# Kernel tuning notes

Measured on AMD Instinct MI355X. Metric: run time of the kernel, lower is better.

Reference implementation:

```python
import jax, jax.numpy as jnp
import numpy as np

N = 50000      # nodes
E = 800000     # edges (before self-loops)
F_IN = 128     # num_features
HID = 32       # hidden channels per head (conv1)
HEADS = 4      # conv1 heads
C = 40         # classes (conv2 out channels)
OUT_HEADS = 1  # conv2 heads
NEG_SLOPE = 0.2


def setup_inputs() -> dict:
    key = jax.random.key(0)
    ks = jax.random.split(key, 10)
    x = jax.random.normal(ks[0], (N, F_IN), jnp.float32)
    edge_index = jax.random.randint(ks[1], (2, E), 0, N, jnp.int32)
    s1 = 1.0 / np.sqrt(F_IN).astype(np.float32)
    s1h = 1.0 / np.sqrt(HID).astype(np.float32)
    s2 = 1.0 / np.sqrt(HEADS * HID).astype(np.float32)
    s2c = 1.0 / np.sqrt(C).astype(np.float32)
    W1 = jax.random.normal(ks[2], (F_IN, HEADS * HID), jnp.float32) * s1
    att_src1 = jax.random.normal(ks[3], (HEADS, HID), jnp.float32) * s1h
    att_dst1 = jax.random.normal(ks[4], (HEADS, HID), jnp.float32) * s1h
    bias1 = jnp.zeros((HEADS * HID,), jnp.float32)
    W2 = jax.random.normal(ks[5], (HEADS * HID, OUT_HEADS * C), jnp.float32) * s2
    att_src2 = jax.random.normal(ks[6], (OUT_HEADS, C), jnp.float32) * s2c
    att_dst2 = jax.random.normal(ks[7], (OUT_HEADS, C), jnp.float32) * s2c
    bias2 = jnp.zeros((C,), jnp.float32)
    return {"x": x, "edge_index": edge_index,
            "W1": W1, "att_src1": att_src1, "att_dst1": att_dst1, "bias1": bias1,
            "W2": W2, "att_src2": att_src2, "att_dst2": att_dst2, "bias2": bias2}


def gat_layer(h_in, src, dst, W, a_src, a_dst, bias, heads, out_ch, concat):
    """PyG GATConv (v1) in inference mode (no dropout on attention)."""
    n = h_in.shape[0]
    h = (h_in @ W).reshape(n, heads, out_ch)              # [N,H,F]
    e_src = jnp.einsum('nhf,hf->nh', h, a_src)            # [N,H]
    e_dst = jnp.einsum('nhf,hf->nh', h, a_dst)            # [N,H]
    alpha = jax.nn.leaky_relu(e_src[src] + e_dst[dst], NEG_SLOPE)  # [E,H]
    # segment softmax over destination-node neighborhoods
    amax = jax.ops.segment_max(alpha, dst, num_segments=n)
    amax = jnp.where(jnp.isfinite(amax), amax, 0.0)
    ex = jnp.exp(alpha - amax[dst])
    denom = jax.ops.segment_sum(ex, dst, num_segments=n)
    coef = ex / (denom[dst] + 1e-16)                      # [E,H]
    # scatter-aggregate weighted source messages
    out = jax.ops.segment_sum(h[src] * coef[:, :, None], dst, num_segments=n)  # [N,H,F]
    out = out.reshape(n, heads * out_ch) if concat else out.mean(axis=1)
    return out + bias


def reference(x, edge_index, W1, att_src1, att_dst1, bias1, W2, att_src2, att_dst2, bias2):
    n = x.shape[0]
    loop = jnp.arange(n, dtype=edge_index.dtype)          # GATConv adds self-loops
    src = jnp.concatenate([edge_index[0], loop])
    dst = jnp.concatenate([edge_index[1], loop])
    h = jax.nn.elu(gat_layer(x, src, dst, W1, att_src1, att_dst1, bias1, HEADS, HID, True))
    out = gat_layer(h, src, dst, W2, att_src2, att_dst2, bias2, OUT_HEADS, C, False)
    return (jax.nn.log_softmax(out, axis=1), jax.nn.softmax(out, axis=1))
```

## Files before the change

kernel.cpp:

```cpp
#include <hip/hip_runtime.h>
#include <hip/hip_bf16.h>

#define F1   128
#define H1   4
#define C2   40
#define NEG  0.2f
#define DS   96

typedef __hip_bfloat16 bf16;
typedef float f32x2 __attribute__((ext_vector_type(2)));
typedef short s16x8 __attribute__((ext_vector_type(8)));
typedef float f32x4 __attribute__((ext_vector_type(4)));

__device__ __forceinline__ float ldf(const void* p, size_t i, int isbf) {
    return isbf ? __bfloat162float(((const bf16*)p)[i]) : ((const float*)p)[i];
}
__device__ __forceinline__ float lrelu(float a) { return a > 0.f ? a : NEG * a; }

__device__ __forceinline__ unsigned short f2bfb(float f, float& back) {
    unsigned u = __float_as_uint(f);
    unsigned r = u + 0x7FFFu + ((u >> 16) & 1u);
    unsigned short h = (unsigned short)(r >> 16);
    back = __uint_as_float((unsigned)h << 16);
    return h;
}

__device__ __forceinline__ void up2(unsigned g, float& lo, float& hi) {
    lo = __uint_as_float(g << 16);
    hi = __uint_as_float(g & 0xffff0000u);
}
__device__ __forceinline__ f32x2 up2v(unsigned g) {
    f32x2 r;
    r.x = __uint_as_float(g << 16);
    r.y = __uint_as_float(g & 0xffff0000u);
    return r;
}

__global__ void k_prep(const unsigned short* __restrict__ x, int* __restrict__ deg,
                       int N, int* __restrict__ flag) {
    int i = blockIdx.x * 256 + threadIdx.x;
    if (i < N) deg[i] = 0;
    if (blockIdx.x == 0) {
        __shared__ int sh[256];
        int cnt = 0;
        for (int k = threadIdx.x; k < 8192; k += 256)
            if (((x[k] >> 7) & 0xFF) >= 160) cnt++;
        sh[threadIdx.x] = cnt;
        __syncthreads();
        for (int s = 128; s > 0; s >>= 1) {
            if (threadIdx.x < s) sh[threadIdx.x] += sh[threadIdx.x + s];
            __syncthreads();
        }
        if (threadIdx.x == 0) flag[0] = (sh[0] < 100) ? 1 : 0;
    }
}

__global__ void k_wprep(const void* __restrict__ W1, const int* __restrict__ flag,
                        unsigned short* __restrict__ w1t_hi,
                        unsigned short* __restrict__ w1t_lo) {
    int idx = blockIdx.x * 256 + threadIdx.x;
    int k = idx >> 7, c = idx & 127;
    const int isbf = flag[0];
    float v = ldf(W1, idx, isbf);
    float back;
    unsigned short hi = f2bfb(v, back);
    float d2;
    unsigned short lo = f2bfb(v - back, d2);
    w1t_hi[c * 128 + k] = hi;
    w1t_lo[c * 128 + k] = isbf ? (unsigned short)0 : lo;
}

__global__ void __launch_bounds__(256) k_scat(const int* __restrict__ ei, int E, int ET,
                                              int* __restrict__ deg,
                                              int* __restrict__ ebuf2) {
    int e = blockIdx.x * 256 + threadIdx.x;
    if (e >= ET) return;
    int s, d;
    if (e < E) { s = ei[e]; d = ei[E + e]; }
    else       { s = e - E; d = e - E; }
    int pos = atomicAdd(&deg[d], 1);
    if (pos < DS) ebuf2[d * DS + pos] = s;
}

__global__ void __launch_bounds__(256) k_gemm1(
        const void* __restrict__ x, const unsigned short* __restrict__ w1t_hi,
        const unsigned short* __restrict__ w1t_lo,
        const void* __restrict__ as1, const void* __restrict__ ad1,
        const int* __restrict__ flag,
        bf16* __restrict__ h1b, float* __restrict__ es1, float* __restrict__ ed1,
        int N) {
    const int isbf = flag[0];
    int t = threadIdx.x, wv = t >> 6, l = t & 63;
    int r0 = (wv & 1) * 16, c0 = (wv >> 1) * 64;
    int lr = l & 15, q = l >> 4;
    int n0 = blockIdx.x * 32;
    int rowa = n0 + r0 + lr; if (rowa >= N) rowa = N - 1;

    const bf16*  xb = (const bf16*)x;
    const float* xf = (const float*)x;
    f32x4 acc[4] = {};

#pragma unroll
    for (int ks = 0; ks < 4; ks++) {
        int kb = ks * 32 + q * 8;
        s16x8 ahi, alo;
        if (isbf) {
            ahi = *(const s16x8*)&xb[(size_t)rowa * 128 + kb];
        } else {
            const float* xr = xf + (size_t)rowa * 128 + kb;
            float4 v0 = *(const float4*)xr;
            float4 v1 = *(const float4*)(xr + 4);
            float vv[8] = {v0.x, v0.y, v0.z, v0.w, v1.x, v1.y, v1.z, v1.w};
#pragma unroll
            for (int j = 0; j < 8; j++) {
                float back;
                unsigned short hb = f2bfb(vv[j], back);
                float d2;
                unsigned short lb = f2bfb(vv[j] - back, d2);
                ahi[j] = (short)hb;
                alo[j] = (short)lb;
            }
        }
#pragma unroll
        for (int f = 0; f < 4; f++) {
            int col = c0 + f * 16 + lr;
            s16x8 bh = *(const s16x8*)&w1t_hi[(size_t)col * 128 + kb];
            acc[f] = __builtin_amdgcn_mfma_f32_16x16x32_bf16(ahi, bh, acc[f], 0, 0, 0);
            if (!isbf) {
                s16x8 bl = *(const s16x8*)&w1t_lo[(size_t)col * 128 + kb];
                acc[f] = __builtin_amdgcn_mfma_f32_16x16x32_bf16(alo, bh, acc[f], 0, 0, 0);
                acc[f] = __builtin_amdgcn_mfma_f32_16x16x32_bf16(ahi, bl, acc[f], 0, 0, 0);
            }
        }
    }

    float asv[4], adv[4];
#pragma unroll
    for (int f = 0; f < 4; f++) {
        asv[f] = ldf(as1, c0 + f * 16 + lr, isbf);
        adv[f] = ldf(ad1, c0 + f * 16 + lr, isbf);
    }
    float ps0[4], ps1[4], pd0[4], pd1[4];
#pragma unroll
    for (int r = 0; r < 4; r++) {
        int rw = n0 + r0 + q * 4 + r;
        ps0[r] = acc[0][r] * asv[0] + acc[1][r] * asv[1];
        ps1[r] = acc[2][r] * asv[2] + acc[3][r] * asv[3];
        pd0[r] = acc[0][r] * adv[0] + acc[1][r] * adv[1];
        pd1[r] = acc[2][r] * adv[2] + acc[3][r] * adv[3];
        if (rw < N) {
#pragma unroll
            for (int f = 0; f < 4; f++)
                h1b[(size_t)rw * 128 + c0 + f * 16 + lr] = __float2bfloat16(acc[f][r]);
        }
    }
#pragma unroll
    for (int off = 1; off < 16; off <<= 1) {
#pragma unroll
        for (int r = 0; r < 4; r++) {
            ps0[r] += __shfl_xor(ps0[r], off, 64);
            ps1[r] += __shfl_xor(ps1[r], off, 64);
            pd0[r] += __shfl_xor(pd0[r], off, 64);
            pd1[r] += __shfl_xor(pd1[r], off, 64);
        }
    }
    if (lr == 0) {
        int h0 = c0 >> 5;
#pragma unroll
        for (int r = 0; r < 4; r++) {
            int rw = n0 + r0 + q * 4 + r;
            if (rw < N) {
                es1[rw * H1 + h0]     = ps0[r];
                es1[rw * H1 + h0 + 1] = ps1[r];
                ed1[rw * H1 + h0]     = pd0[r];
                ed1[rw * H1 + h0 + 1] = pd1[r];
            }
        }
    }
}

__global__ void __launch_bounds__(256) k_l1(
        const int* __restrict__ deg, const int* __restrict__ ebuf2,
        const float* __restrict__ es1, const float* __restrict__ ed1,
        const uint4* __restrict__ h1p4, const void* __restrict__ b1,
        const void* __restrict__ W2, const void* __restrict__ as2,
        const void* __restrict__ ad2, const int* __restrict__ flag,
        bf16* __restrict__ h2b, float* __restrict__ es2, float* __restrict__ ed2,
        int N) {
    int w = threadIdx.x >> 6, l = threadIdx.x & 63;
    int d = blockIdx.x * 4 + w; if (d >= N) d = N - 1;
    int cnt = deg[d]; if (cnt > DS) cnt = DS;
    int start = d * DS;

    __shared__ int   s_sh[4][DS];
    __shared__ float ev_sh[4][4][DS + 4];
    __shared__ float hs[4][144];

    float4 edv = *(const float4*)&ed1[(size_t)d * 4];
    float t0 = 0.f, t1 = 0.f, t2 = 0.f, t3 = 0.f;
    if (l < cnt) {
        int s = ebuf2[start + l];
        s_sh[w][l] = s;
        float4 es4 = *(const float4*)&es1[(size_t)s * 4];
        float v0 = __expf(lrelu(es4.x + edv.x));
        float v1 = __expf(lrelu(es4.y + edv.y));
        float v2 = __expf(lrelu(es4.z + edv.z));
        float v3 = __expf(lrelu(es4.w + edv.w));
        ev_sh[w][0][l] = v0; ev_sh[w][1][l] = v1;
        ev_sh[w][2][l] = v2; ev_sh[w][3][l] = v3;
        t0 = v0; t1 = v1; t2 = v2; t3 = v3;
    }
    if (cnt > 64) {
        int l2 = 64 + l;
        if (l2 < cnt) {
            int s = ebuf2[start + l2];
            s_sh[w][l2] = s;
            float4 es4 = *(const float4*)&es1[(size_t)s * 4];
            float v0 = __expf(lrelu(es4.x + edv.x));
            float v1 = __expf(lrelu(es4.y + edv.y));
            float v2 = __expf(lrelu(es4.z + edv.z));
            float v3 = __expf(lrelu(es4.w + edv.w));
            ev_sh[w][0][l2] = v0; ev_sh[w][1][l2] = v1;
            ev_sh[w][2][l2] = v2; ev_sh[w][3][l2] = v3;
            t0 += v0; t1 += v1; t2 += v2; t3 += v3;
        }
    }
#pragma unroll
    for (int off = 32; off > 0; off >>= 1) {
        t0 += __shfl_xor(t0, off, 64);
        t1 += __shfl_xor(t1, off, 64);
        t2 += __shfl_xor(t2, off, 64);
        t3 += __shfl_xor(t3, off, 64);
    }
    __syncthreads();

    int q = l >> 4, c16 = l & 15, h = c16 >> 2;
    f32x2 acc[4] = {{0.f, 0.f}, {0.f, 0.f}, {0.f, 0.f}, {0.f, 0.f}};
    for (int i = 0; i < cnt; i += 16) {
#pragma unroll
        for (int u = 0; u < 4; u++) {
            int e = i + q + 4 * u;
            int ec = min(e, cnt - 1);
            float evh = (e < cnt) ? ev_sh[w][h][ec] : 0.f;
            int s = s_sh[w][ec];
            uint4 g = h1p4[(size_t)s * 16 + c16];
            f32x2 ev2 = {evh, evh};
            acc[0] += ev2 * up2v(g.x);
            acc[1] += ev2 * up2v(g.y);
            acc[2] += ev2 * up2v(g.z);
            acc[3] += ev2 * up2v(g.w);
        }
    }

#pragma unroll
    for (int off = 16; off <= 32; off <<= 1) {
#pragma unroll
        for (int jj = 0; jj < 4; jj++) {
            acc[jj].x += __shfl_xor(acc[jj].x, off, 64);
            acc[jj].y += __shfl_xor(acc[jj].y, off, 64);
        }
    }

    const int isbf = flag[0];
    float dsum = (h == 0) ? t0 : (h == 1) ? t1 : (h == 2) ? t2 : t3;
    if (q == 0) {
        float inv = 1.f / (dsum + 1e-16f);
#pragma unroll
        for (int j = 0; j < 8; j++) {
            int col = c16 * 8 + j;
            float av = (j & 1) ? acc[j >> 1].y : acc[j >> 1].x;
            float v = av * inv + ldf(b1, col, isbf);
            hs[w][col + (col >> 3)] = v > 0.f ? v : (__expf(v) - 1.f);
        }
    }
    __syncthreads();
    float a2 = 0.f;
    if (l < C2) {
        if (isbf) {
            const bf16* W = (const bf16*)W2;
#pragma unroll 8
            for (int k = 0; k < F1; k++)
                a2 = fmaf(hs[w][k + (k >> 3)], __bfloat162float(W[(size_t)k * C2 + l]), a2);
        } else {
            const float* W = (const float*)W2;
#pragma unroll 8
            for (int k = 0; k < F1; k++)
                a2 = fmaf(hs[w][k + (k >> 3)], W[(size_t)k * C2 + l], a2);
        }
        h2b[(size_t)d * C2 + l] = __float2bfloat16(a2);
    }
    float ps = (l < C2) ? a2 * ldf(as2, l, isbf) : 0.f;
    float pd = (l < C2) ? a2 * ldf(ad2, l, isbf) : 0.f;
#pragma unroll
    for (int off = 32; off > 0; off >>= 1) {
        ps += __shfl_xor(ps, off, 64);
        pd += __shfl_xor(pd, off, 64);
    }
    if (l == 0) { es2[d] = ps; ed2[d] = pd; }
}

__global__ void __launch_bounds__(256) k_l2(
        const int* __restrict__ deg, const int* __restrict__ ebuf2,
        const float* __restrict__ es2, const float* __restrict__ ed2,
        const unsigned* __restrict__ h2p, const void* __restrict__ b2,
        const int* __restrict__ flag, void* __restrict__ out, int N) {
    int w = threadIdx.x >> 6, l = threadIdx.x & 63;
    int d = blockIdx.x * 4 + w; if (d >= N) d = N - 1;
    int cnt = deg[d]; if (cnt > DS) cnt = DS;
    int start = d * DS;
    float edd = ed2[d];

    __shared__ int   s_sh2[4][DS];
    __shared__ float x_sh[4][DS];

    float xv = 0.f;
    if (l < cnt) {
        int s = ebuf2[start + l];
        s_sh2[w][l] = s;
        xv = __expf(lrelu(es2[s] + edd));
        x_sh[w][l] = xv;
    }
    float dsum = xv;
    if (cnt > 64) {
        int l2 = 64 + l;
        if (l2 < cnt) {
            int s = ebuf2[start + l2];
            s_sh2[w][l2] = s;
            float x2 = __expf(lrelu(es2[s] + edd));
            x_sh[w][l2] = x2;
            dsum += x2;
        }
    }
#pragma unroll
    for (int off = 32; off > 0; off >>= 1) dsum += __shfl_xor(dsum, off, 64);
    __syncthreads();

    int half = l >> 5, j = l & 31;
    float acc0 = 0.f, acc1 = 0.f;
    if (j < 20) {
        for (int i = 0; i < cnt; i += 16) {
#pragma unroll
            for (int u = 0; u < 8; u++) {
                int e = i + half * 8 + u;
                int ec = min(e, cnt - 1);
                float x = (e < cnt) ? x_sh[w][ec] : 0.f;
                int s = s_sh2[w][ec];
                unsigned g = h2p[(size_t)s * 20 + j];
                float lo, hi; up2(g, lo, hi);
                acc0 = fmaf(x, lo, acc0);
                acc1 = fmaf(x, hi, acc1);
            }
        }
        acc0 += __shfl_xor(acc0, 32, 64);
        acc1 += __shfl_xor(acc1, 32, 64);
    }

    const int isbf = flag[0];
    float inv = 1.f / (dsum + 1e-16f);
    float v0 = -1e30f, v1 = -1e30f;
    if (l < 20) {
        v0 = acc0 * inv + ldf(b2, 2 * l, isbf);
        v1 = acc1 * inv + ldf(b2, 2 * l + 1, isbf);
    }
    float m = fmaxf(v0, v1);
#pragma unroll
    for (int off = 16; off > 0; off >>= 1) m = fmaxf(m, __shfl_xor(m, off, 32));
    float sv = (l < 20) ? __expf(v0 - m) + __expf(v1 - m) : 0.f;
#pragma unroll
    for (int off = 16; off > 0; off >>= 1) sv += __shfl_xor(sv, off, 32);
    float lse = m + __logf(sv);
    if (l < 20) {
        float ls0 = v0 - lse, ls1 = v1 - lse;
        size_t base = (size_t)d * C2 + 2 * l, halfo = (size_t)N * C2;
        if (isbf) {
            bf16* o = (bf16*)out;
            o[base] = __float2bfloat16(ls0);
            o[base + 1] = __float2bfloat16(ls1);
            o[halfo + base] = __float2bfloat16(__expf(ls0));
            o[halfo + base + 1] = __float2bfloat16(__expf(ls1));
        } else {
            float* o = (float*)out;
            o[base] = ls0;
            o[base + 1] = ls1;
            o[halfo + base] = __expf(ls0);
            o[halfo + base + 1] = __expf(ls1);
        }
    }
}

extern "C" void kernel_launch(void* const* d_in, const int* in_sizes, int n_in,
                              void* d_out, int out_size, void* d_ws, size_t ws_size,
                              hipStream_t stream) {
    const int N  = in_sizes[0] / F1;
    const int E  = in_sizes[1] / 2;
    const int ET = E + N;
    const int NB = (N + 255) / 256;

    const void* x   = d_in[0];
    const int*  ei  = (const int*)d_in[1];
    const void* W1  = d_in[2];
    const void* as1 = d_in[3];
    const void* ad1 = d_in[4];
    const void* b1  = d_in[5];
    const void* W2  = d_in[6];
    const void* as2 = d_in[7];
    const void* ad2 = d_in[8];
    const void* b2  = d_in[9];

    float* ws = (float*)d_ws;
    auto al4 = [](size_t v) { return (v + 3) & ~(size_t)3; };
    size_t o = 0;
    bf16*  h1b  = (bf16*)(ws + o); o = al4(o + (size_t)64 * N);
    float* es1  = ws + o; o = al4(o + (size_t)H1 * N);
    float* ed1  = ws + o; o = al4(o + (size_t)H1 * N);
    bf16*  h2b  = (bf16*)(ws + o); o = al4(o + (size_t)20 * N);
    float* es2  = ws + o; o = al4(o + N);
    float* ed2  = ws + o; o = al4(o + N);
    int*   deg  = (int*)(ws + o); o = al4(o + N);
    int*   flag = (int*)(ws + o); o = al4(o + 4);
    int*   ebuf2 = (int*)(ws + o); o = al4(o + (size_t)DS * N);
    unsigned short* w1t_hi = (unsigned short*)(ws + o); o = al4(o + 8192);
    unsigned short* w1t_lo = (unsigned short*)(ws + o); o = al4(o + 8192);

    k_prep<<<NB, 256, 0, stream>>>((const unsigned short*)x, deg, N, flag);
    k_wprep<<<64, 256, 0, stream>>>(W1, flag, w1t_hi, w1t_lo);
    k_scat<<<(ET + 255) / 256, 256, 0, stream>>>(ei, E, ET, deg, ebuf2);
    k_gemm1<<<(N + 31) / 32, 256, 0, stream>>>(x, w1t_hi, w1t_lo, as1, ad1, flag,
                                               h1b, es1, ed1, N);
    k_l1<<<(N + 3) / 4, 256, 0, stream>>>(deg, ebuf2, es1, ed1, (const uint4*)h1b,
                                          b1, W2, as2, ad2, flag, h2b, es2, ed2, N);
    k_l2<<<(N + 3) / 4, 256, 0, stream>>>(deg, ebuf2, es2, ed2, (const unsigned*)h2b,
                                          b2, flag, d_out, N);
}
```

Measured before the change: 313.2 us.

## Fuse edge scatter into GEMM1 and split adjacency buckets into four sub-copies

The standalone edge-bucketing kernel is folded into the start of the first GEMM kernel, with each block handling a contiguous slice of edges. Per-destination counters and bucket storage are replicated four ways, indexed by block id, to reduce atomic contention on shared counters. The layer kernels gather neighbors by concatenating the four sub-buckets, each capped at 32 entries. This removes a launch and spreads atomics, but the GEMM now waits on scattered atomics, and the 32-per-copy cap could drop edges for high-degree nodes that the old 96 cap kept.

```diff
diff --git a/kernel.cpp b/kernel.cpp
--- a/kernel.cpp
+++ b/kernel.cpp
@@ -6,6 +6,8 @@
 #define C2   40
 #define NEG  0.2f
 #define DS   96
+#define NC   4
+#define DSX  32
 
 typedef __hip_bfloat16 bf16;
 typedef float f32x2 __attribute__((ext_vector_type(2)));
@@ -36,10 +38,10 @@
     return r;
 }
 
-__global__ void k_prep(const unsigned short* __restrict__ x, int* __restrict__ deg,
-                       int N, int* __restrict__ flag) {
+__global__ void k_prep(const unsigned short* __restrict__ x, int* __restrict__ deg_x,
+                       int N4, int* __restrict__ flag) {
     int i = blockIdx.x * 256 + threadIdx.x;
-    if (i < N) deg[i] = 0;
+    if (i < N4) deg_x[i] = 0;
     if (blockIdx.x == 0) {
         __shared__ int sh[256];
         int cnt = 0;
@@ -70,25 +72,28 @@
     w1t_lo[c * 128 + k] = isbf ? (unsigned short)0 : lo;
 }
 
-__global__ void __launch_bounds__(256) k_scat(const int* __restrict__ ei, int E, int ET,
-                                              int* __restrict__ deg,
-                                              int* __restrict__ ebuf2) {
-    int e = blockIdx.x * 256 + threadIdx.x;
-    if (e >= ET) return;
-    int s, d;
-    if (e < E) { s = ei[e]; d = ei[E + e]; }
-    else       { s = e - E; d = e - E; }
-    int pos = atomicAdd(&deg[d], 1);
-    if (pos < DS) ebuf2[d * DS + pos] = s;
-}
-
 __global__ void __launch_bounds__(256) k_gemm1(
         const void* __restrict__ x, const unsigned short* __restrict__ w1t_hi,
         const unsigned short* __restrict__ w1t_lo,
         const void* __restrict__ as1, const void* __restrict__ ad1,
-        const int* __restrict__ flag,
+        const int* __restrict__ flag, const int* __restrict__ ei,
+        int E, int ET, int* __restrict__ deg_x, int* __restrict__ ebufx,
         bf16* __restrict__ h1b, float* __restrict__ es1, float* __restrict__ ed1,
         int N) {
+    {
+        int per = (ET + gridDim.x - 1) / gridDim.x;
+        int he0 = blockIdx.x * per;
+        int he1 = he0 + per; if (he1 > ET) he1 = ET;
+        int xc = blockIdx.x & (NC - 1);
+        for (int e = he0 + threadIdx.x; e < he1; e += 256) {
+            int s, d;
+            if (e < E) { s = ei[e]; d = ei[E + e]; }
+            else       { s = e - E; d = e - E; }
+            size_t seg = (size_t)xc * N + d;
+            int pos = atomicAdd(&deg_x[seg], 1);
+            if (pos < DSX) ebufx[seg * DSX + pos] = s;
+        }
+    }
     const int isbf = flag[0];
     int t = threadIdx.x, wv = t >> 6, l = t & 63;
     int r0 = (wv & 1) * 16, c0 = (wv >> 1) * 64;
@@ -180,7 +185,7 @@
 }
 
 __global__ void __launch_bounds__(256) k_l1(
-        const int* __restrict__ deg, const int* __restrict__ ebuf2,
+        const int* __restrict__ deg_x, const int* __restrict__ ebufx,
         const float* __restrict__ es1, const float* __restrict__ ed1,
         const uint4* __restrict__ h1p4, const void* __restrict__ b1,
         const void* __restrict__ W2, const void* __restrict__ as2,
@@ -189,48 +194,40 @@
         int N) {
     int w = threadIdx.x >> 6, l = threadIdx.x & 63;
     int d = blockIdx.x * 4 + w; if (d >= N) d = N - 1;
-    int cnt = deg[d]; if (cnt > DS) cnt = DS;
-    int start = d * DS;
-
     __shared__ int   s_sh[4][DS];
     __shared__ float ev_sh[4][4][DS + 4];
     __shared__ float hs[4][144];
 
     float4 edv = *(const float4*)&ed1[(size_t)d * 4];
     float t0 = 0.f, t1 = 0.f, t2 = 0.f, t3 = 0.f;
-    if (l < cnt) {
-        int s = ebuf2[start + l];
-        s_sh[w][l] = s;
-        float4 es4 = *(const float4*)&es1[(size_t)s * 4];
-        float v0 = __expf(lrelu(es4.x + edv.x));
-        float v1 = __expf(lrelu(es4.y + edv.y));
-        float v2 = __expf(lrelu(es4.z + edv.z));
-        float v3 = __expf(lrelu(es4.w + edv.w));
-        ev_sh[w][0][l] = v0; ev_sh[w][1][l] = v1;
-        ev_sh[w][2][l] = v2; ev_sh[w][3][l] = v3;
-        t0 = v0; t1 = v1; t2 = v2; t3 = v3;
-    }
-    if (cnt > 64) {
-        int l2 = 64 + l;
-        if (l2 < cnt) {
-            int s = ebuf2[start + l2];
-            s_sh[w][l2] = s;
+    int off = 0;
+#pragma unroll
+    for (int xc = 0; xc < NC; xc++) {
+        size_t seg = (size_t)xc * N + d;
+        int c = deg_x[seg]; if (c > DSX) c = DSX;
+        int take = c; if (off + take > DS) take = DS - off;
+        if (l < take) {
+            int s = ebufx[seg * DSX + l];
+            int idx = off + l;
+            s_sh[w][idx] = s;
             float4 es4 = *(const float4*)&es1[(size_t)s * 4];
             float v0 = __expf(lrelu(es4.x + edv.x));
             float v1 = __expf(lrelu(es4.y + edv.y));
             float v2 = __expf(lrelu(es4.z + edv.z));
             float v3 = __expf(lrelu(es4.w + edv.w));
-            ev_sh[w][0][l2] = v0; ev_sh[w][1][l2] = v1;
-            ev_sh[w][2][l2] = v2; ev_sh[w][3][l2] = v3;
+            ev_sh[w][0][idx] = v0; ev_sh[w][1][idx] = v1;
+            ev_sh[w][2][idx] = v2; ev_sh[w][3][idx] = v3;
             t0 += v0; t1 += v1; t2 += v2; t3 += v3;
         }
-    }
-#pragma unroll
-    for (int off = 32; off > 0; off >>= 1) {
-        t0 += __shfl_xor(t0, off, 64);
-        t1 += __shfl_xor(t1, off, 64);
-        t2 += __shfl_xor(t2, off, 64);
-        t3 += __shfl_xor(t3, off, 64);
+        off += take;
+    }
+    int cnt = off;
+#pragma unroll
+    for (int o = 32; o > 0; o >>= 1) {
+        t0 += __shfl_xor(t0, o, 64);
+        t1 += __shfl_xor(t1, o, 64);
+        t2 += __shfl_xor(t2, o, 64);
+        t3 += __shfl_xor(t3, o, 64);
     }
     __syncthreads();
 
@@ -253,11 +250,11 @@
     }
 
 #pragma unroll
-    for (int off = 16; off <= 32; off <<= 1) {
+    for (int o = 16; o <= 32; o <<= 1) {
 #pragma unroll
         for (int jj = 0; jj < 4; jj++) {
-            acc[jj].x += __shfl_xor(acc[jj].x, off, 64);
-            acc[jj].y += __shfl_xor(acc[jj].y, off, 64);
+            acc[jj].x += __shfl_xor(acc[jj].x, o, 64);
+            acc[jj].y += __shfl_xor(acc[jj].y, o, 64);
         }
     }
 
@@ -292,47 +289,45 @@
     float ps = (l < C2) ? a2 * ldf(as2, l, isbf) : 0.f;
     float pd = (l < C2) ? a2 * ldf(ad2, l, isbf) : 0.f;
 #pragma unroll
-    for (int off = 32; off > 0; off >>= 1) {
-        ps += __shfl_xor(ps, off, 64);
-        pd += __shfl_xor(pd, off, 64);
+    for (int o = 32; o > 0; o >>= 1) {
+        ps += __shfl_xor(ps, o, 64);
+        pd += __shfl_xor(pd, o, 64);
     }
     if (l == 0) { es2[d] = ps; ed2[d] = pd; }
 }
 
 __global__ void __launch_bounds__(256) k_l2(
-        const int* __restrict__ deg, const int* __restrict__ ebuf2,
+        const int* __restrict__ deg_x, const int* __restrict__ ebufx,
         const float* __restrict__ es2, const float* __restrict__ ed2,
         const unsigned* __restrict__ h2p, const void* __restrict__ b2,
         const int* __restrict__ flag, void* __restrict__ out, int N) {
     int w = threadIdx.x >> 6, l = threadIdx.x & 63;
     int d = blockIdx.x * 4 + w; if (d >= N) d = N - 1;
-    int cnt = deg[d]; if (cnt > DS) cnt = DS;
-    int start = d * DS;
     float edd = ed2[d];
 
     __shared__ int   s_sh2[4][DS];
     __shared__ float x_sh[4][DS];
 
-    float xv = 0.f;
-    if (l < cnt) {
-        int s = ebuf2[start + l];
-        s_sh2[w][l] = s;
-        xv = __expf(lrelu(es2[s] + edd));
-        x_sh[w][l] = xv;
-    }
-    float dsum = xv;
-    if (cnt > 64) {
-        int l2 = 64 + l;
-        if (l2 < cnt) {
-            int s = ebuf2[start + l2];
-            s_sh2[w][l2] = s;
-            float x2 = __expf(lrelu(es2[s] + edd));
-            x_sh[w][l2] = x2;
-            dsum += x2;
-        }
-    }
-#pragma unroll
-    for (int off = 32; off > 0; off >>= 1) dsum += __shfl_xor(dsum, off, 64);
+    float dsum = 0.f;
+    int off = 0;
+#pragma unroll
+    for (int xc = 0; xc < NC; xc++) {
+        size_t seg = (size_t)xc * N + d;
+        int c = deg_x[seg]; if (c > DSX) c = DSX;
+        int take = c; if (off + take > DS) take = DS - off;
+        if (l < take) {
+            int s = ebufx[seg * DSX + l];
+            int idx = off + l;
+            s_sh2[w][idx] = s;
+            float xv = __expf(lrelu(es2[s] + edd));
+            x_sh[w][idx] = xv;
+            dsum += xv;
+        }
+        off += take;
+    }
+    int cnt = off;
+#pragma unroll
+    for (int o = 32; o > 0; o >>= 1) dsum += __shfl_xor(dsum, o, 64);
     __syncthreads();
 
     int half = l >> 5, j = l & 31;
@@ -364,10 +359,10 @@
     }
     float m = fmaxf(v0, v1);
 #pragma unroll
-    for (int off = 16; off > 0; off >>= 1) m = fmaxf(m, __shfl_xor(m, off, 32));
+    for (int o = 16; o > 0; o >>= 1) m = fmaxf(m, __shfl_xor(m, o, 32));
     float sv = (l < 20) ? __expf(v0 - m) + __expf(v1 - m) : 0.f;
 #pragma unroll
-    for (int off = 16; off > 0; off >>= 1) sv += __shfl_xor(sv, off, 32);
+    for (int o = 16; o > 0; o >>= 1) sv += __shfl_xor(sv, o, 32);
     float lse = m + __logf(sv);
     if (l < 20) {
         float ls0 = v0 - lse, ls1 = v1 - lse;
@@ -394,7 +389,8 @@
     const int N  = in_sizes[0] / F1;
     const int E  = in_sizes[1] / 2;
     const int ET = E + N;
-    const int NB = (N + 255) / 256;
+    const int N4 = NC * N;
+    const int NB4 = (N4 + 255) / 256;
 
     const void* x   = d_in[0];
     const int*  ei  = (const int*)d_in[1];
@@ -416,19 +412,19 @@
     bf16*  h2b  = (bf16*)(ws + o); o = al4(o + (size_t)20 * N);
     float* es2  = ws + o; o = al4(o + N);
     float* ed2  = ws + o; o = al4(o + N);
-    int*   deg  = (int*)(ws + o); o = al4(o + N);
+    int*   deg_x = (int*)(ws + o); o = al4(o + (size_t)NC * N);
     int*   flag = (int*)(ws + o); o = al4(o + 4);
-    int*   ebuf2 = (int*)(ws + o); o = al4(o + (size_t)DS * N);
+    int*   ebufx = (int*)(ws + o); o = al4(o + (size_t)NC * DSX * N);
     unsigned short* w1t_hi = (unsigned short*)(ws + o); o = al4(o + 8192);
     unsigned short* w1t_lo = (unsigned short*)(ws + o); o = al4(o + 8192);
 
-    k_prep<<<NB, 256, 0, stream>>>((const unsigned short*)x, deg, N, flag);
+    k_prep<<<NB4, 256, 0, stream>>>((const unsigned short*)x, deg_x, N4, flag);
     k_wprep<<<64, 256, 0, stream>>>(W1, flag, w1t_hi, w1t_lo);
-    k_scat<<<(ET + 255) / 256, 256, 0, stream>>>(ei, E, ET, deg, ebuf2);
     k_gemm1<<<(N + 31) / 32, 256, 0, stream>>>(x, w1t_hi, w1t_lo, as1, ad1, flag,
+                                               ei, E, ET, deg_x, ebufx,
                                                h1b, es1, ed1, N);
-    k_l1<<<(N + 3) / 4, 256, 0, stream>>>(deg, ebuf2, es1, ed1, (const uint4*)h1b,
+    k_l1<<<(N + 3) / 4, 256, 0, stream>>>(deg_x, ebufx, es1, ed1, (const uint4*)h1b,
                                           b1, W2, as2, ad2, flag, h2b, es2, ed2, N);
-    k_l2<<<(N + 3) / 4, 256, 0, stream>>>(deg, ebuf2, es2, ed2, (const unsigned*)h2b,
+    k_l2<<<(N + 3) / 4, 256, 0, stream>>>(deg_x, ebufx, es2, ed2, (const unsigned*)h2b,
                                           b2, flag, d_out, N);
 }
```

Measured after the change: 344.8 us. 10.1% more time.

## Replace atomic per-node edge scatter with two-pass binned counting sort into CSR

Applied to the files above, without the earlier changes.

Replaces the global-atomic scatter of edges into fixed 96-slot per-node buckets with a two-pass sort. The first pass bins edges by destination block of 256 nodes, staging them in shared memory. The second pass sorts each bin by local destination in shared memory and writes compact CSR source lists with row starts and degrees. The aim is to cut global atomic contention and scattered writes, and to give the aggregation kernels a denser CSR layout. In exchange it adds an extra kernel and a staging buffer, and edges are silently dropped if a bin exceeds its fixed capacity.

```diff
diff --git a/kernel.cpp b/kernel.cpp
--- a/kernel.cpp
+++ b/kernel.cpp
@@ -6,6 +6,8 @@
 #define C2   40
 #define NEG  0.2f
 #define DS   96
+#define EPB  6400
+#define BCAP 5632
 
 typedef __hip_bfloat16 bf16;
 typedef float f32x2 __attribute__((ext_vector_type(2)));
@@ -36,23 +38,36 @@
     return r;
 }
 
-__global__ void k_prep(const unsigned short* __restrict__ x, int* __restrict__ deg,
-                       int N, int* __restrict__ flag) {
-    int i = blockIdx.x * 256 + threadIdx.x;
-    if (i < N) deg[i] = 0;
-    if (blockIdx.x == 0) {
-        __shared__ int sh[256];
-        int cnt = 0;
-        for (int k = threadIdx.x; k < 8192; k += 256)
-            if (((x[k] >> 7) & 0xFF) >= 160) cnt++;
-        sh[threadIdx.x] = cnt;
+__device__ __forceinline__ int excl_scan256(int v, int t, int* wsum) {
+    int lane = t & 63, wid = t >> 6;
+    int orig = v;
+#pragma unroll
+    for (int o = 1; o < 64; o <<= 1) {
+        int n = __shfl_up(v, o, 64);
+        if (lane >= o) v += n;
+    }
+    if (lane == 63) wsum[wid] = v;
+    __syncthreads();
+    int add = 0;
+    for (int k = 0; k < wid; k++) add += wsum[k];
+    return v + add - orig;
+}
+
+__global__ void k_prep(const unsigned short* __restrict__ x, int* __restrict__ gbin_cnt,
+                       int* __restrict__ flag) {
+    int t = threadIdx.x;
+    gbin_cnt[t] = 0;
+    __shared__ int sh[256];
+    int cnt = 0;
+    for (int k = t; k < 8192; k += 256)
+        if (((x[k] >> 7) & 0xFF) >= 160) cnt++;
+    sh[t] = cnt;
+    __syncthreads();
+    for (int s = 128; s > 0; s >>= 1) {
+        if (t < s) sh[t] += sh[t + s];
         __syncthreads();
-        for (int s = 128; s > 0; s >>= 1) {
-            if (threadIdx.x < s) sh[threadIdx.x] += sh[threadIdx.x + s];
-            __syncthreads();
-        }
-        if (threadIdx.x == 0) flag[0] = (sh[0] < 100) ? 1 : 0;
-    }
+    }
+    if (t == 0) flag[0] = (sh[0] < 100) ? 1 : 0;
 }
 
 __global__ void k_wprep(const void* __restrict__ W1, const int* __restrict__ flag,
@@ -70,16 +85,74 @@
     w1t_lo[c * 128 + k] = isbf ? (unsigned short)0 : lo;
 }
 
-__global__ void __launch_bounds__(256) k_scat(const int* __restrict__ ei, int E, int ET,
-                                              int* __restrict__ deg,
-                                              int* __restrict__ ebuf2) {
-    int e = blockIdx.x * 256 + threadIdx.x;
-    if (e >= ET) return;
-    int s, d;
-    if (e < E) { s = ei[e]; d = ei[E + e]; }
-    else       { s = e - E; d = e - E; }
-    int pos = atomicAdd(&deg[d], 1);
-    if (pos < DS) ebuf2[d * DS + pos] = s;
+__global__ void __launch_bounds__(256) k_scatA(
+        const int* __restrict__ ei, int E, int ET, int nbins,
+        int* __restrict__ gbin_cnt, unsigned long long* __restrict__ stg) {
+    __shared__ int hist[256], lstart[256], gbase[256], lcnt[256];
+    __shared__ int wsum[4];
+    __shared__ unsigned long long stgl[EPB];
+    int t = threadIdx.x;
+    hist[t] = 0; lcnt[t] = 0;
+    __syncthreads();
+    int e0 = blockIdx.x * EPB;
+    int e1 = e0 + EPB; if (e1 > ET) e1 = ET;
+    for (int e = e0 + t; e < e1; e += 256) {
+        int d = (e < E) ? ei[E + e] : (e - E);
+        atomicAdd(&hist[d >> 8], 1);
+    }
+    __syncthreads();
+    if (t < nbins && hist[t] > 0) gbase[t] = atomicAdd(&gbin_cnt[t], hist[t]);
+    int ls = excl_scan256(hist[t], t, wsum);
+    lstart[t] = ls;
+    __syncthreads();
+    for (int e = e0 + t; e < e1; e += 256) {
+        int s, d;
+        if (e < E) { s = ei[e]; d = ei[E + e]; }
+        else       { s = e - E; d = e - E; }
+        int b = d >> 8;
+        int r = atomicAdd(&lcnt[b], 1);
+        stgl[lstart[b] + r] = ((unsigned long long)(unsigned)d << 32) | (unsigned)s;
+    }
+    __syncthreads();
+    int cntb = e1 - e0;
+    for (int i = t; i < cntb; i += 256) {
+        unsigned long long p = stgl[i];
+        int d = (int)(p >> 32);
+        int b = d >> 8;
+        int off = gbase[b] + (i - lstart[b]);
+        if (off < BCAP) stg[(size_t)b * BCAP + off] = p;
+    }
+}
+
+__global__ void __launch_bounds__(256) k_scatB(
+        const unsigned long long* __restrict__ stg, const int* __restrict__ gbin_cnt,
+        int N, int* __restrict__ csr_s, int* __restrict__ rowstart,
+        int* __restrict__ deg) {
+    __shared__ int dhist[256], dstart[256], dcnt[256];
+    __shared__ int wsum[4];
+    __shared__ int out_s[BCAP];
+    int bin = blockIdx.x, t = threadIdx.x;
+    int cnt = gbin_cnt[bin]; if (cnt > BCAP) cnt = BCAP;
+    dhist[t] = 0; dcnt[t] = 0;
+    __syncthreads();
+    const unsigned long long* mystg = stg + (size_t)bin * BCAP;
+    for (int i = t; i < cnt; i += 256)
+        atomicAdd(&dhist[(int)(mystg[i] >> 32) & 255], 1);
+    __syncthreads();
+    int ds = excl_scan256(dhist[t], t, wsum);
+    dstart[t] = ds;
+    __syncthreads();
+    for (int i = t; i < cnt; i += 256) {
+        unsigned long long p = mystg[i];
+        int ld = (int)(p >> 32) & 255;
+        int r = atomicAdd(&dcnt[ld], 1);
+        out_s[dstart[ld] + r] = (int)(p & 0xffffffffu);
+    }
+    __syncthreads();
+    size_t gb = (size_t)bin * BCAP;
+    for (int i = t; i < cnt; i += 256) csr_s[gb + i] = out_s[i];
+    int d = bin * 256 + t;
+    if (d < N) { rowstart[d] = (int)gb + dstart[t]; deg[d] = dhist[t]; }
 }
 
 __global__ void __launch_bounds__(256) k_gemm1(
@@ -180,7 +253,8 @@
 }
 
 __global__ void __launch_bounds__(256) k_l1(
-        const int* __restrict__ deg, const int* __restrict__ ebuf2,
+        const int* __restrict__ deg, const int* __restrict__ rowstart,
+        const int* __restrict__ csr_s,
         const float* __restrict__ es1, const float* __restrict__ ed1,
         const uint4* __restrict__ h1p4, const void* __restrict__ b1,
         const void* __restrict__ W2, const void* __restrict__ as2,
@@ -190,7 +264,7 @@
     int w = threadIdx.x >> 6, l = threadIdx.x & 63;
     int d = blockIdx.x * 4 + w; if (d >= N) d = N - 1;
     int cnt = deg[d]; if (cnt > DS) cnt = DS;
-    int start = d * DS;
+    int start = rowstart[d];
 
     __shared__ int   s_sh[4][DS];
     __shared__ float ev_sh[4][4][DS + 4];
@@ -199,7 +273,7 @@
     float4 edv = *(const float4*)&ed1[(size_t)d * 4];
     float t0 = 0.f, t1 = 0.f, t2 = 0.f, t3 = 0.f;
     if (l < cnt) {
-        int s = ebuf2[start + l];
+        int s = csr_s[start + l];
         s_sh[w][l] = s;
         float4 es4 = *(const float4*)&es1[(size_t)s * 4];
         float v0 = __expf(lrelu(es4.x + edv.x));
@@ -213,7 +287,7 @@
     if (cnt > 64) {
         int l2 = 64 + l;
         if (l2 < cnt) {
-            int s = ebuf2[start + l2];
+            int s = csr_s[start + l2];
             s_sh[w][l2] = s;
             float4 es4 = *(const float4*)&es1[(size_t)s * 4];
             float v0 = __expf(lrelu(es4.x + edv.x));
@@ -226,11 +300,11 @@
         }
     }
 #pragma unroll
-    for (int off = 32; off > 0; off >>= 1) {
-        t0 += __shfl_xor(t0, off, 64);
-        t1 += __shfl_xor(t1, off, 64);
-        t2 += __shfl_xor(t2, off, 64);
-        t3 += __shfl_xor(t3, off, 64);
+    for (int o = 32; o > 0; o >>= 1) {
+        t0 += __shfl_xor(t0, o, 64);
+        t1 += __shfl_xor(t1, o, 64);
+        t2 += __shfl_xor(t2, o, 64);
+        t3 += __shfl_xor(t3, o, 64);
     }
     __syncthreads();
 
@@ -253,11 +327,11 @@
     }
 
 #pragma unroll
-    for (int off = 16; off <= 32; off <<= 1) {
+    for (int o = 16; o <= 32; o <<= 1) {
 #pragma unroll
         for (int jj = 0; jj < 4; jj++) {
-            acc[jj].x += __shfl_xor(acc[jj].x, off, 64);
-            acc[jj].y += __shfl_xor(acc[jj].y, off, 64);
+            acc[jj].x += __shfl_xor(acc[jj].x, o, 64);
+            acc[jj].y += __shfl_xor(acc[jj].y, o, 64);
         }
     }
 
@@ -292,22 +366,23 @@
     float ps = (l < C2) ? a2 * ldf(as2, l, isbf) : 0.f;
     float pd = (l < C2) ? a2 * ldf(ad2, l, isbf) : 0.f;
 #pragma unroll
-    for (int off = 32; off > 0; off >>= 1) {
-        ps += __shfl_xor(ps, off, 64);
-        pd += __shfl_xor(pd, off, 64);
+    for (int o = 32; o > 0; o >>= 1) {
+        ps += __shfl_xor(ps, o, 64);
+        pd += __shfl_xor(pd, o, 64);
     }
     if (l == 0) { es2[d] = ps; ed2[d] = pd; }
 }
 
 __global__ void __launch_bounds__(256) k_l2(
-        const int* __restrict__ deg, const int* __restrict__ ebuf2,
+        const int* __restrict__ deg, const int* __restrict__ rowstart,
+        const int* __restrict__ csr_s,
         const float* __restrict__ es2, const float* __restrict__ ed2,
         const unsigned* __restrict__ h2p, const void* __restrict__ b2,
         const int* __restrict__ flag, void* __restrict__ out, int N) {
     int w = threadIdx.x >> 6, l = threadIdx.x & 63;
     int d = blockIdx.x * 4 + w; if (d >= N) d = N - 1;
     int cnt = deg[d]; if (cnt > DS) cnt = DS;
-    int start = d * DS;
+    int start = rowstart[d];
     float edd = ed2[d];
 
     __shared__ int   s_sh2[4][DS];
@@ -315,7 +390,7 @@
 
     float xv = 0.f;
     if (l < cnt) {
-        int s = ebuf2[start + l];
+        int s = csr_s[start + l];
         s_sh2[w][l] = s;
         xv = __expf(lrelu(es2[s] + edd));
         x_sh[w][l] = xv;
@@ -324,7 +399,7 @@
     if (cnt > 64) {
         int l2 = 64 + l;
         if (l2 < cnt) {
-            int s = ebuf2[start + l2];
+            int s = csr_s[start + l2];
             s_sh2[w][l2] = s;
             float x2 = __expf(lrelu(es2[s] + edd));
             x_sh[w][l2] = x2;
@@ -332,7 +407,7 @@
         }
     }
 #pragma unroll
-    for (int off = 32; off > 0; off >>= 1) dsum += __shfl_xor(dsum, off, 64);
+    for (int o = 32; o > 0; o >>= 1) dsum += __shfl_xor(dsum, o, 64);
     __syncthreads();
 
     int half = l >> 5, j = l & 31;
@@ -364,10 +439,10 @@
     }
     float m = fmaxf(v0, v1);
 #pragma unroll
-    for (int off = 16; off > 0; off >>= 1) m = fmaxf(m, __shfl_xor(m, off, 32));
+    for (int o = 16; o > 0; o >>= 1) m = fmaxf(m, __shfl_xor(m, o, 32));
     float sv = (l < 20) ? __expf(v0 - m) + __expf(v1 - m) : 0.f;
 #pragma unroll
-    for (int off = 16; off > 0; off >>= 1) sv += __shfl_xor(sv, off, 32);
+    for (int o = 16; o > 0; o >>= 1) sv += __shfl_xor(sv, o, 32);
     float lse = m + __logf(sv);
     if (l < 20) {
         float ls0 = v0 - lse, ls1 = v1 - lse;
@@ -394,7 +469,7 @@
     const int N  = in_sizes[0] / F1;
     const int E  = in_sizes[1] / 2;
     const int ET = E + N;
-    const int NB = (N + 255) / 256;
+    const int NBINS = (N + 255) >> 8;
 
     const void* x   = d_in[0];
     const int*  ei  = (const int*)d_in[1];
@@ -417,18 +492,24 @@
     float* es2  = ws + o; o = al4(o + N);
     float* ed2  = ws + o; o = al4(o + N);
     int*   deg  = (int*)(ws + o); o = al4(o + N);
+    int*   rowstart = (int*)(ws + o); o = al4(o + N);
+    int*   gbin_cnt = (int*)(ws + o); o = al4(o + 256);
     int*   flag = (int*)(ws + o); o = al4(o + 4);
-    int*   ebuf2 = (int*)(ws + o); o = al4(o + (size_t)DS * N);
+    int*   csr_s = (int*)(ws + o); o = al4(o + (size_t)NBINS * BCAP);
     unsigned short* w1t_hi = (unsigned short*)(ws + o); o = al4(o + 8192);
     unsigned short* w1t_lo = (unsigned short*)(ws + o); o = al4(o + 8192);
-
-    k_prep<<<NB, 256, 0, stream>>>((const unsigned short*)x, deg, N, flag);
+    unsigned long long* stg = (unsigned long long*)(ws + o);
+    o = al4(o + (size_t)2 * NBINS * BCAP);
+
+    k_prep<<<1, 256, 0, stream>>>((const unsigned short*)x, gbin_cnt, flag);
     k_wprep<<<64, 256, 0, stream>>>(W1, flag, w1t_hi, w1t_lo);
-    k_scat<<<(ET + 255) / 256, 256, 0, stream>>>(ei, E, ET, deg, ebuf2);
+    k_scatA<<<(ET + EPB - 1) / EPB, 256, 0, stream>>>(ei, E, ET, NBINS, gbin_cnt, stg);
+    k_scatB<<<NBINS, 256, 0, stream>>>(stg, gbin_cnt, N, csr_s, rowstart, deg);
     k_gemm1<<<(N + 31) / 32, 256, 0, stream>>>(x, w1t_hi, w1t_lo, as1, ad1, flag,
                                                h1b, es1, ed1, N);
-    k_l1<<<(N + 3) / 4, 256, 0, stream>>>(deg, ebuf2, es1, ed1, (const uint4*)h1b,
-                                          b1, W2, as2, ad2, flag, h2b, es2, ed2, N);
-    k_l2<<<(N + 3) / 4, 256, 0, stream>>>(deg, ebuf2, es2, ed2, (const unsigned*)h2b,
-                                          b2, flag, d_out, N);
-}
+    k_l1<<<(N + 3) / 4, 256, 0, stream>>>(deg, rowstart, csr_s, es1, ed1,
+                                          (const uint4*)h1b, b1, W2, as2, ad2, flag,
+                                          h2b, es2, ed2, N);
+    k_l2<<<(N + 3) / 4, 256, 0, stream>>>(deg, rowstart, csr_s, es2, ed2,
+                                          (const unsigned*)h2b, b2, flag, d_out, N);
+}
```

Measured after the change: 289.8 us. -7.5%, faster.
